# Kernel tuning notes

Measured on AMD Instinct MI355X. Metric: run time of the kernel, lower is better.

Reference implementation:

```python
import jax, jax.numpy as jnp
import numpy as np

C, H, W = 16, 512, 512
HID = 128
N_STEPS = 8


def setup_inputs() -> dict:
    key = jax.random.key(0)
    k1, k2, k3 = jax.random.split(key, 3)
    state = jax.random.normal(k1, (C, H, W), dtype=jnp.float32)
    # MLP params: 5*C = 80 gathered features -> HID -> C delta channels
    W1 = jax.random.normal(k2, (5 * C, HID), dtype=jnp.float32) * (1.0 / np.sqrt(5 * C))
    b1 = jnp.zeros((HID,), dtype=jnp.float32)
    W2 = jax.random.normal(k3, (HID, C), dtype=jnp.float32) * (1.0 / np.sqrt(HID))
    b2 = jnp.zeros((C,), dtype=jnp.float32)
    return {"state": state, "W1": W1, "b1": b1, "W2": W2, "b2": b2, "n_steps": N_STEPS}


def _neighbor_idx(n):
    i = jnp.arange(n)
    minus = jnp.maximum(i - 1, 0)          # clamp at low edge (cy==0 -> 0)
    plus = jnp.where(i == n - 1, 0, i + 1)  # WRAP to 0 at high edge (original quirk)
    return minus, plus


def reference(state, W1, b1, W2, b2, n_steps):
    c, h, w = state.shape
    up, down = _neighbor_idx(h)
    left, right = _neighbor_idx(w)

    def step(s, _):
        # von-Neumann gather: (5C, H, W), feature order [center, up, down, left, right]
        feats = jnp.concatenate(
            [s, s[:, up, :], s[:, down, :], s[:, :, left], s[:, :, right]], axis=0)
        x = feats.reshape(5 * c, h * w).T        # (HW, 5C)
        hdn = jax.nn.relu(x @ W1 + b1)           # (HW, HID)
        delta = (hdn @ W2 + b2).T.reshape(c, h, w)
        s_new = s + delta
        s_new = s_new.at[0].set(s[0])            # channel 0 snapshot restore
        return s_new, None

    out, _ = jax.lax.scan(step, state, None, length=n_steps)
    return out
```

## Files before the change

kernel.cpp:

```cpp
#include <hip/hip_runtime.h>
#include <hip/hip_bf16.h>

#define HH 512
#define WW 512
#define CC 16
#define HIDN 128
#define HWSZ (HH*WW)

typedef __attribute__((ext_vector_type(8))) short short8;
typedef __attribute__((ext_vector_type(4))) short short4v;
typedef __attribute__((ext_vector_type(4))) float float4v;

__device__ __forceinline__ short to_bf16(float f){
    __hip_bfloat16 h = __float2bfloat16(f);
    return __builtin_bit_cast(short, h);
}

#define RSTRIDE 24
#define RROW    (68*RSTRIDE)

__global__ void __launch_bounds__(256) prep_kernel(
    const float* __restrict__ W1, const float* __restrict__ W2,
    short* __restrict__ w1t, short* __restrict__ w2t)
{
    int t = blockIdx.x * blockDim.x + threadIdx.x;
    int stride = gridDim.x * blockDim.x;
    for (int idx = t; idx < HIDN*96; idx += stride){
        int n = idx / 96;
        int k = idx - n*96;
        float v = (k < 80) ? W1[k*HIDN + n] : 0.0f;
        w1t[idx] = to_bf16(v);
    }
    for (int idx = t; idx < CC*HIDN; idx += stride){
        int n = idx >> 7;
        int k = idx & 127;
        w2t[idx] = to_bf16(W2[k*CC + n]);
    }
}

__global__ void __launch_bounds__(256, 5) step_kernel(
    const float* __restrict__ src, float* __restrict__ dst,
    const short* __restrict__ w1t, const short* __restrict__ w2t,
    const float* __restrict__ b1, const float* __restrict__ b2)
{
    __shared__ __align__(16) short rows_u[3*RROW];
    __shared__ __align__(16) short hdn[64][136];
    __shared__ float b1s[HIDN];
    __shared__ float b2s[CC];
    float (*stg)[65] = (float (*)[65])rows_u;

    const int t    = threadIdx.x;
    const int w    = t >> 6;
    const int lane = t & 63;
    const int ln15 = lane & 15;
    const int g4   = lane >> 4;

    const int bid = blockIdx.x;
    const int xcd = bid & 7;
    const int i   = bid >> 3;
    const int y   = (xcd << 6) + (i >> 3);
    const int xs  = (i & 7) << 6;

    const int yu = (y == 0)      ? 0 : (y - 1);
    const int yd = (y == HH - 1) ? 0 : (y + 1);

    float res[4];
    #pragma unroll
    for (int ii = 0; ii < 4; ++ii){
        const int idx = t + (ii << 8);
        const int c2  = idx >> 6;
        const int xo  = idx & 63;
        res[ii] = src[(size_t)c2 * HWSZ + (size_t)y * WW + xs + xo];
    }

    if (t < HIDN) b1s[t] = b1[t];
    if (t < CC)   b2s[t] = b2[t];

    if (t < 192){
        const int r  = t >> 6;
        const int l  = t & 63;
        const int q  = l & 15;
        const int cq = l >> 4;
        const int rowg = (r == 0) ? y : ((r == 1) ? yu : yd);
        const float* base = src + (size_t)rowg * WW + xs + (q << 2);
        float4v f[4];
        #pragma unroll
        for (int ii = 0; ii < 4; ++ii)
            f[ii] = *(const float4v*)(base + (size_t)((cq << 2) + ii) * HWSZ);
        #pragma unroll
        for (int j = 0; j < 4; ++j){
            const int xl   = (q << 2) + 1 + j;
            const int key  = (xl >> 3) & 1;
            const int slot = (cq >> 1) ^ key;
            short4v v;
            v[0] = to_bf16(f[0][j]); v[1] = to_bf16(f[1][j]);
            v[2] = to_bf16(f[2][j]); v[3] = to_bf16(f[3][j]);
            *(short4v*)&rows_u[r*RROW + xl*RSTRIDE + (slot << 3) + ((cq & 1) << 2)] = v;
        }
    } else if (t < 224){
        const int c    = (t - 192) & 15;
        const int side = (t - 192) >> 4;
        const int gx   = (side == 0) ? ((xs == 0) ? 0 : xs - 1)
                                     : ((xs + 64 == WW) ? 0 : xs + 64);
        rows_u[(side * 65)*RSTRIDE + c] =
            to_bf16(src[(size_t)c*HWSZ + (size_t)y*WW + gx]);
    }
    __syncthreads();

    int offA[3];
    #pragma unroll
    for (int kk = 0; kk < 3; ++kk){
        const int g  = (kk < 2) ? ((kk << 2) + g4) : (8 + (g4 & 1));
        const int n  = g >> 1;
        const int oc = g & 1;
        const int r  = (n == 1) ? 1 : ((n == 2) ? 2 : 0);
        const int dx = (n == 3) ? -1 : ((n == 4) ? 1 : 0);
        const int xl = ln15 + 1 + dx;
        const int key = (xl >> 3) & 1;
        offA[kk] = r*RROW + xl*RSTRIDE + ((oc ^ key) << 3);
    }

    const int wm = w & 1, wn = w >> 1;
    float4v acc[2][4];
    #pragma unroll
    for (int mt = 0; mt < 2; ++mt)
        #pragma unroll
        for (int nt = 0; nt < 4; ++nt)
            acc[mt][nt] = (float4v){0.f, 0.f, 0.f, 0.f};

    #pragma unroll
    for (int kk = 0; kk < 3; ++kk){
        short8 bfrag[4];
        #pragma unroll
        for (int nt = 0; nt < 4; ++nt){
            const int col = (wn << 6) + (nt << 4) + ln15;
            bfrag[nt] = *(const short8*)(w1t + col * 96 + (kk << 5) + (g4 << 3));
        }
        #pragma unroll
        for (int mt = 0; mt < 2; ++mt){
            short8 afrag = *(const short8*)(&rows_u[offA[kk] + ((wm << 5) + (mt << 4)) * RSTRIDE]);
            #pragma unroll
            for (int nt = 0; nt < 4; ++nt){
                acc[mt][nt] = __builtin_amdgcn_mfma_f32_16x16x32_bf16(
                    afrag, bfrag[nt], acc[mt][nt], 0, 0, 0);
            }
        }
    }

    #pragma unroll
    for (int nt = 0; nt < 4; ++nt){
        const int col  = (wn << 6) + (nt << 4) + ln15;
        const float bias = b1s[col];
        #pragma unroll
        for (int mt = 0; mt < 2; ++mt){
            #pragma unroll
            for (int r = 0; r < 4; ++r){
                const int m = (wm << 5) + (mt << 4) + (g4 << 2) + r;
                float v = acc[mt][nt][r] + bias;
                v = v > 0.f ? v : 0.f;
                hdn[m][col] = to_bf16(v);
            }
        }
    }
    __syncthreads();

    float4v acc2 = (float4v){0.f, 0.f, 0.f, 0.f};
    #pragma unroll
    for (int kk = 0; kk < 4; ++kk){
        short8 a = *(const short8*)(&hdn[(w << 4) + ln15][(kk << 5) + (g4 << 3)]);
        short8 b = *(const short8*)(w2t + ln15 * HIDN + (kk << 5) + (g4 << 3));
        acc2 = __builtin_amdgcn_mfma_f32_16x16x32_bf16(a, b, acc2, 0, 0, 0);
    }

    {
        const int c = ln15;
        const float bias2 = b2s[c];
        const int p0 = (w << 4) + (g4 << 2);
        #pragma unroll
        for (int r = 0; r < 4; ++r)
            stg[c][p0 + r] = acc2[r] + bias2;
    }
    __syncthreads();

    #pragma unroll
    for (int ii = 0; ii < 4; ++ii){
        const int idx = t + (ii << 8);
        const int c2  = idx >> 6;
        const int xo  = idx & 63;
        float v = res[ii];
        if (c2 != 0) v += stg[c2][xo];
        dst[(size_t)c2 * HWSZ + (size_t)y * WW + xs + xo] = v;
    }
}

extern "C" void kernel_launch(void* const* d_in, const int* in_sizes, int n_in,
                              void* d_out, int out_size, void* d_ws, size_t ws_size,
                              hipStream_t stream)
{
    const float* state = (const float*)d_in[0];
    const float* W1    = (const float*)d_in[1];
    const float* b1    = (const float*)d_in[2];
    const float* W2    = (const float*)d_in[3];
    const float* b2    = (const float*)d_in[4];

    float* B1  = (float*)d_ws;
    short* w1t = (short*)((char*)d_ws + (size_t)HWSZ * CC * 4);
    short* w2t = w1t + HIDN * 96;
    float* out = (float*)d_out;

    prep_kernel<<<32, 256, 0, stream>>>(W1, W2, w1t, w2t);

    dim3 grid(HH * (WW / 64));
    step_kernel<<<grid, 256, 0, stream>>>(state, B1, w1t, w2t, b1, b2);
    step_kernel<<<grid, 256, 0, stream>>>(B1, out, w1t, w2t, b1, b2);
    step_kernel<<<grid, 256, 0, stream>>>(out, B1, w1t, w2t, b1, b2);
    step_kernel<<<grid, 256, 0, stream>>>(B1, out, w1t, w2t, b1, b2);
    step_kernel<<<grid, 256, 0, stream>>>(out, B1, w1t, w2t, b1, b2);
    step_kernel<<<grid, 256, 0, stream>>>(B1, out, w1t, w2t, b1, b2);
    step_kernel<<<grid, 256, 0, stream>>>(out, B1, w1t, w2t, b1, b2);
    step_kernel<<<grid, 256, 0, stream>>>(B1, out, w1t, w2t, b1, b2);
}
```

Baseline: 284.7 us.

## Keep hidden activations in registers via identity-MFMA transpose, drop LDS round trip

The hidden layer is no longer written to shared memory and read back. Each wave transposes its first-GEMM accumulator fragments with an identity-matrix MFMA and feeds them directly into 16x16x16 MFMAs against a repacked W2, producing partial outputs per column-half that are summed in a small staging buffer. This removes one __syncthreads and the hdn LDS array, cuts shared memory use and raises the launch-bounds occupancy target. In exchange it adds extra MFMAs and conversions, plus an extra bf16 rounding of the hidden values through the identity product; biases are now loaded into registers.

```diff
diff --git a/kernel.cpp b/kernel.cpp
--- a/kernel.cpp
+++ b/kernel.cpp
@@ -16,12 +16,9 @@
     return __builtin_bit_cast(short, h);
 }
 
-#define RSTRIDE 24
-#define RROW    (68*RSTRIDE)
-
 __global__ void __launch_bounds__(256) prep_kernel(
     const float* __restrict__ W1, const float* __restrict__ W2,
-    short* __restrict__ w1t, short* __restrict__ w2t)
+    short* __restrict__ w1t, short* __restrict__ w2q)
 {
     int t = blockIdx.x * blockDim.x + threadIdx.x;
     int stride = gridDim.x * blockDim.x;
@@ -31,29 +28,32 @@
         float v = (k < 80) ? W1[k*HIDN + n] : 0.0f;
         w1t[idx] = to_bf16(v);
     }
-    for (int idx = t; idx < CC*HIDN; idx += stride){
-        int n = idx >> 7;
-        int k = idx & 127;
-        w2t[idx] = to_bf16(W2[k*CC + n]);
-    }
-}
-
-__global__ void __launch_bounds__(256, 5) step_kernel(
+    for (int idx = t; idx < HIDN*CC; idx += stride){
+        int j  = idx & 3;
+        int c  = (idx >> 2) & 15;
+        int hq = idx >> 6;
+        int hid = (hq << 2) | j;
+        w2q[idx] = to_bf16(W2[hid*CC + c]);
+    }
+}
+
+#define RSTRIDE 24
+#define RROW    (68*RSTRIDE)
+
+__global__ void __launch_bounds__(256, 6) step_kernel(
     const float* __restrict__ src, float* __restrict__ dst,
-    const short* __restrict__ w1t, const short* __restrict__ w2t,
+    const short* __restrict__ w1t, const short* __restrict__ w2q,
     const float* __restrict__ b1, const float* __restrict__ b2)
 {
     __shared__ __align__(16) short rows_u[3*RROW];
-    __shared__ __align__(16) short hdn[64][136];
-    __shared__ float b1s[HIDN];
-    __shared__ float b2s[CC];
-    float (*stg)[65] = (float (*)[65])rows_u;
+    __shared__ __align__(16) float stg2[2][16][68];
 
     const int t    = threadIdx.x;
     const int w    = t >> 6;
     const int lane = t & 63;
     const int ln15 = lane & 15;
     const int g4   = lane >> 4;
+    const int wm   = w & 1, wn = w >> 1;
 
     const int bid = blockIdx.x;
     const int xcd = bid & 7;
@@ -67,14 +67,17 @@
     float res[4];
     #pragma unroll
     for (int ii = 0; ii < 4; ++ii){
-        const int idx = t + (ii << 8);
-        const int c2  = idx >> 6;
-        const int xo  = idx & 63;
-        res[ii] = src[(size_t)c2 * HWSZ + (size_t)y * WW + xs + xo];
-    }
-
-    if (t < HIDN) b1s[t] = b1[t];
-    if (t < CC)   b2s[t] = b2[t];
+        const int c2 = w + (ii << 2);
+        res[ii] = src[(size_t)c2 * HWSZ + (size_t)y * WW + xs + lane];
+    }
+    float bias1[4];
+    #pragma unroll
+    for (int nt = 0; nt < 4; ++nt)
+        bias1[nt] = b1[(wn << 6) + (nt << 4) + ln15];
+    float b2v[4];
+    #pragma unroll
+    for (int ii = 0; ii < 4; ++ii)
+        b2v[ii] = b2[w + (ii << 2)];
 
     if (t < 192){
         const int r  = t >> 6;
@@ -120,7 +123,6 @@
         offA[kk] = r*RROW + xl*RSTRIDE + ((oc ^ key) << 3);
     }
 
-    const int wm = w & 1, wn = w >> 1;
     float4v acc[2][4];
     #pragma unroll
     for (int mt = 0; mt < 2; ++mt)
@@ -147,49 +149,54 @@
         }
     }
 
+    short4v idf;
+    #pragma unroll
+    for (int j = 0; j < 4; ++j)
+        idf[j] = ((g4 << 2) + j == ln15) ? (short)0x3F80 : (short)0;
+
+    short4v b2f[4];
     #pragma unroll
     for (int nt = 0; nt < 4; ++nt){
-        const int col  = (wn << 6) + (nt << 4) + ln15;
-        const float bias = b1s[col];
+        const int hq = (wn << 4) + (nt << 2) + g4;
+        b2f[nt] = *(const short4v*)(w2q + (hq << 6) + (ln15 << 2));
+    }
+
+    float4v acc2[2];
+    acc2[0] = (float4v){0.f, 0.f, 0.f, 0.f};
+    acc2[1] = (float4v){0.f, 0.f, 0.f, 0.f};
+    #pragma unroll
+    for (int nt = 0; nt < 4; ++nt){
         #pragma unroll
         for (int mt = 0; mt < 2; ++mt){
+            short4v af;
             #pragma unroll
             for (int r = 0; r < 4; ++r){
-                const int m = (wm << 5) + (mt << 4) + (g4 << 2) + r;
-                float v = acc[mt][nt][r] + bias;
+                float v = acc[mt][nt][r] + bias1[nt];
                 v = v > 0.f ? v : 0.f;
-                hdn[m][col] = to_bf16(v);
+                af[r] = to_bf16(v);
             }
-        }
-    }
+            float4v tt = __builtin_amdgcn_mfma_f32_16x16x16bf16_1k(
+                af, idf, (float4v){0.f, 0.f, 0.f, 0.f}, 0, 0, 0);
+            short4v a2;
+            #pragma unroll
+            for (int j = 0; j < 4; ++j)
+                a2[j] = to_bf16(tt[j]);
+            acc2[mt] = __builtin_amdgcn_mfma_f32_16x16x16bf16_1k(
+                a2, b2f[nt], acc2[mt], 0, 0, 0);
+        }
+    }
+
+    #pragma unroll
+    for (int mt = 0; mt < 2; ++mt)
+        *(float4v*)&stg2[wn][ln15][(wm << 5) + (mt << 4) + (g4 << 2)] = acc2[mt];
     __syncthreads();
 
-    float4v acc2 = (float4v){0.f, 0.f, 0.f, 0.f};
-    #pragma unroll
-    for (int kk = 0; kk < 4; ++kk){
-        short8 a = *(const short8*)(&hdn[(w << 4) + ln15][(kk << 5) + (g4 << 3)]);
-        short8 b = *(const short8*)(w2t + ln15 * HIDN + (kk << 5) + (g4 << 3));
-        acc2 = __builtin_amdgcn_mfma_f32_16x16x32_bf16(a, b, acc2, 0, 0, 0);
-    }
-
-    {
-        const int c = ln15;
-        const float bias2 = b2s[c];
-        const int p0 = (w << 4) + (g4 << 2);
-        #pragma unroll
-        for (int r = 0; r < 4; ++r)
-            stg[c][p0 + r] = acc2[r] + bias2;
-    }
-    __syncthreads();
-
     #pragma unroll
     for (int ii = 0; ii < 4; ++ii){
-        const int idx = t + (ii << 8);
-        const int c2  = idx >> 6;
-        const int xo  = idx & 63;
+        const int c2 = w + (ii << 2);
         float v = res[ii];
-        if (c2 != 0) v += stg[c2][xo];
-        dst[(size_t)c2 * HWSZ + (size_t)y * WW + xs + xo] = v;
+        if (c2 != 0) v += stg2[0][c2][lane] + stg2[1][c2][lane] + b2v[ii];
+        dst[(size_t)c2 * HWSZ + (size_t)y * WW + xs + lane] = v;
     }
 }
 
@@ -205,18 +212,18 @@
 
     float* B1  = (float*)d_ws;
     short* w1t = (short*)((char*)d_ws + (size_t)HWSZ * CC * 4);
-    short* w2t = w1t + HIDN * 96;
+    short* w2q = w1t + HIDN * 96;
     float* out = (float*)d_out;
 
-    prep_kernel<<<32, 256, 0, stream>>>(W1, W2, w1t, w2t);
+    prep_kernel<<<32, 256, 0, stream>>>(W1, W2, w1t, w2q);
 
     dim3 grid(HH * (WW / 64));
-    step_kernel<<<grid, 256, 0, stream>>>(state, B1, w1t, w2t, b1, b2);
-    step_kernel<<<grid, 256, 0, stream>>>(B1, out, w1t, w2t, b1, b2);
-    step_kernel<<<grid, 256, 0, stream>>>(out, B1, w1t, w2t, b1, b2);
-    step_kernel<<<grid, 256, 0, stream>>>(B1, out, w1t, w2t, b1, b2);
-    step_kernel<<<grid, 256, 0, stream>>>(out, B1, w1t, w2t, b1, b2);
-    step_kernel<<<grid, 256, 0, stream>>>(B1, out, w1t, w2t, b1, b2);
-    step_kernel<<<grid, 256, 0, stream>>>(out, B1, w1t, w2t, b1, b2);
-    step_kernel<<<grid, 256, 0, stream>>>(B1, out, w1t, w2t, b1, b2);
-}
+    step_kernel<<<grid, 256, 0, stream>>>(state, B1, w1t, w2q, b1, b2);
+    step_kernel<<<grid, 256, 0, stream>>>(B1, out, w1t, w2q, b1, b2);
+    step_kernel<<<grid, 256, 0, stream>>>(out, B1, w1t, w2q, b1, b2);
+    step_kernel<<<grid, 256, 0, stream>>>(B1, out, w1t, w2q, b1, b2);
+    step_kernel<<<grid, 256, 0, stream>>>(out, B1, w1t, w2q, b1, b2);
+    step_kernel<<<grid, 256, 0, stream>>>(B1, out, w1t, w2q, b1, b2);
+    step_kernel<<<grid, 256, 0, stream>>>(out, B1, w1t, w2q, b1, b2);
+    step_kernel<<<grid, 256, 0, stream>>>(B1, out, w1t, w2q, b1, b2);
+}
```

After: 331.9 us. 1.17x slower.
